# Optimization experiments

Measured on AMD Instinct MI355X. Metric: run time of the kernel, lower is better.

The kernel has to match this reference:

```python
import jax, jax.numpy as jnp
import numpy as np

N_VERTS = 500000
M_MASK = 250000
C_FEAT = 128
K_ORDER = 20000


def setup_inputs() -> dict:
    key = jax.random.key(0)
    k1, k2 = jax.random.split(key)
    img = jax.random.normal(k1, (M_MASK, C_FEAT), dtype=jnp.float32)
    # boolean mask in the original selects M_MASK rows; expressed as unique int indices
    mask_idx = jnp.arange(M_MASK, dtype=jnp.int64)
    order = jax.random.randint(k2, (2, K_ORDER), 0, N_VERTS, dtype=jnp.int64)
    return {"img": img, "mask_idx": mask_idx, "order": order, "num_vertices": N_VERTS}


def reference(img, mask_idx, order, num_vertices):
    # v_f = zeros(N, C); v_f[mask] = img
    v_f = jnp.zeros((num_vertices, img.shape[1]), dtype=img.dtype).at[mask_idx].set(img)
    # sequential copy chain, replayed in reverse column order:
    #   for idx in range(K): t = order[1, K-1-idx]; f = order[0, K-1-idx]; v_f[t] = v_f[f]
    cols = order[:, ::-1].T  # [K, 2] rows of (f, t), last column first
    def step(v, col):
        f, t = col[0], col[1]
        return v.at[t].set(v[f]), None
    v_f, _ = jax.lax.scan(step, v_f, cols)
    return v_f
```

## Files before the change

### kernel.cpp

```cpp
#include <hip/hip_runtime.h>


__global__ void init_kernel(int* __restrict__ LW, int* __restrict__ inv,
                            int* __restrict__ head, int N) {
    int r = blockIdx.x * blockDim.x + threadIdx.x;
    if (r < N) { LW[r] = -1; inv[r] = -1; head[r] = -1; }
}

__global__ void scatter_inv(const int* __restrict__ mask_idx, int* __restrict__ inv, int M) {
    int i = blockIdx.x * blockDim.x + threadIdx.x;
    if (i < M) inv[mask_idx[i]] = i;
}

__global__ void lw_chain_kernel(const int* __restrict__ order, int K,
                                int* __restrict__ LW, int* __restrict__ head,
                                int* __restrict__ next) {
    int s = blockIdx.x * blockDim.x + threadIdx.x;
    if (s < K) {
        int t = order[2 * K - 1 - s];
        atomicMax(&LW[t], s);
        next[s] = atomicExch(&head[t], s);
    }
}

__global__ void parent_kernel(const int* __restrict__ order, int K,
                              const int* __restrict__ head, const int* __restrict__ next,
                              int* __restrict__ parent) {
    int s = blockIdx.x * blockDim.x + threadIdx.x;
    if (s >= K) return;
    int f = order[K - 1 - s];
    int best = -1;
    for (int cur = head[f]; cur >= 0; cur = next[cur])
        if (cur < s && cur > best) best = cur;
    parent[s] = (best >= 0) ? best : s;
}

__global__ void res_kernel(const int* __restrict__ order, int K,
                           const int* __restrict__ parent, int* __restrict__ RES) {
    int s = blockIdx.x * blockDim.x + threadIdx.x;
    if (s >= K) return;
    int cur = s;
    int p = parent[cur];
    while (p != cur) { cur = p; p = parent[cur]; }
    RES[s] = order[K - 1 - cur];
}

__global__ void out_kernel(const float4* __restrict__ img4, const int* __restrict__ LW,
                           const int* __restrict__ inv, const int* __restrict__ RES,
                           float4* __restrict__ out4, int N, int c4shift) {
    int C4 = 1 << c4shift;
    int rowsPerBlock = blockDim.x >> c4shift;
    int row = blockIdx.x * rowsPerBlock + (threadIdx.x >> c4shift);
    int c4 = threadIdx.x & (C4 - 1);
    if (row >= N) return;
    int lw = LW[row];
    int src = (lw < 0) ? row : RES[lw];
    int j = inv[src];
    float4 val = make_float4(0.f, 0.f, 0.f, 0.f);
    if (j >= 0) val = img4[(long)j * C4 + c4];
    out4[(long)row * C4 + c4] = val;
}

extern "C" void kernel_launch(void* const* d_in, const int* in_sizes, int n_in,
                              void* d_out, int out_size, void* d_ws, size_t ws_size,
                              hipStream_t stream) {
    const float* img      = (const float*)d_in[0];
    const int*   mask_idx = (const int*)d_in[1];
    const int*   order    = (const int*)d_in[2];
    float*       out      = (float*)d_out;

    const int M  = in_sizes[1];
    const int C  = in_sizes[0] / M;
    const int K  = in_sizes[2] / 2;
    const int N  = out_size / C;
    const int C4 = C / 4;
    int c4shift = 0;
    while ((1 << c4shift) < C4) ++c4shift;

    int* LW     = (int*)d_ws;
    int* inv    = LW + N;
    int* head   = inv + N;
    int* next   = head + N;
    int* parent = next + K;
    int* RES    = parent + K;

    const int B = 256;

    init_kernel<<<(N + B - 1) / B, B, 0, stream>>>(LW, inv, head, N);
    scatter_inv<<<(M + B - 1) / B, B, 0, stream>>>(mask_idx, inv, M);
    lw_chain_kernel<<<(K + B - 1) / B, B, 0, stream>>>(order, K, LW, head, next);
    parent_kernel<<<(K + B - 1) / B, B, 0, stream>>>(order, K, head, next, parent);
    res_kernel<<<(K + B - 1) / B, B, 0, stream>>>(order, K, parent, RES);

    int rowsPerBlock = B >> c4shift;
    out_kernel<<<(N + rowsPerBlock - 1) / rowsPerBlock, B, 0, stream>>>(
        (const float4*)img, LW, inv, RES, (float4*)out, N, c4shift);
}
```

Before: 368.6 us.

## Split output into bulk stream plus sparse fix-up of copied rows

Reworks the pipeline from six kernels to four. Only the vertices touched by `order` are initialised, scatter and chain-building are fused into one kernel, and the output is first written as a plain masked copy. A sparse fix-up kernel then overwrites only the last-written target rows, walking each copy chain inline instead of building parent/RES arrays. This removes full-N passes over LW/head and the per-row LW/RES indirection in the big output kernel. In exchange, the chain resolution is redone per target in the fix-up kernel, and correctness depends on that kernel being ordered after the bulk stream.

```diff
diff --git a/kernel.cpp b/kernel.cpp
--- a/kernel.cpp
+++ b/kernel.cpp
@@ -1,64 +1,75 @@
 #include <hip/hip_runtime.h>
 
 
-__global__ void init_kernel(int* __restrict__ LW, int* __restrict__ inv,
-                            int* __restrict__ head, int N) {
-    int r = blockIdx.x * blockDim.x + threadIdx.x;
-    if (r < N) { LW[r] = -1; inv[r] = -1; head[r] = -1; }
-}
-
-__global__ void scatter_inv(const int* __restrict__ mask_idx, int* __restrict__ inv, int M) {
+__global__ __launch_bounds__(256) void k1_init(const int* __restrict__ order, int K,
+                                               int* __restrict__ inv, int* __restrict__ LW,
+                                               int* __restrict__ head, int N) {
     int i = blockIdx.x * blockDim.x + threadIdx.x;
-    if (i < M) inv[mask_idx[i]] = i;
-}
-
-__global__ void lw_chain_kernel(const int* __restrict__ order, int K,
-                                int* __restrict__ LW, int* __restrict__ head,
-                                int* __restrict__ next) {
-    int s = blockIdx.x * blockDim.x + threadIdx.x;
-    if (s < K) {
-        int t = order[2 * K - 1 - s];
-        atomicMax(&LW[t], s);
-        next[s] = atomicExch(&head[t], s);
+    if (i < N) inv[i] = -1;
+    if (i < K) {
+        int f = order[K - 1 - i];
+        int t = order[2 * K - 1 - i];
+        LW[t] = -1;
+        head[t] = -1;
+        head[f] = -1;
     }
 }
 
-__global__ void parent_kernel(const int* __restrict__ order, int K,
-                              const int* __restrict__ head, const int* __restrict__ next,
-                              int* __restrict__ parent) {
-    int s = blockIdx.x * blockDim.x + threadIdx.x;
-    if (s >= K) return;
-    int f = order[K - 1 - s];
-    int best = -1;
-    for (int cur = head[f]; cur >= 0; cur = next[cur])
-        if (cur < s && cur > best) best = cur;
-    parent[s] = (best >= 0) ? best : s;
+__global__ __launch_bounds__(256) void k2_build(const int* __restrict__ mask_idx, int M,
+                                                const int* __restrict__ order, int K,
+                                                int* __restrict__ inv, int* __restrict__ LW,
+                                                int* __restrict__ head, int* __restrict__ next) {
+    int i = blockIdx.x * blockDim.x + threadIdx.x;
+    if (i < M) inv[mask_idx[i]] = i;
+    if (i < K) {
+        int t = order[2 * K - 1 - i];
+        atomicMax(&LW[t], i);
+        next[i] = atomicExch(&head[t], i);
+    }
 }
 
-__global__ void res_kernel(const int* __restrict__ order, int K,
-                           const int* __restrict__ parent, int* __restrict__ RES) {
-    int s = blockIdx.x * blockDim.x + threadIdx.x;
-    if (s >= K) return;
-    int cur = s;
-    int p = parent[cur];
-    while (p != cur) { cur = p; p = parent[cur]; }
-    RES[s] = order[K - 1 - cur];
+__global__ __launch_bounds__(256) void k3_stream(const float4* __restrict__ img4,
+                                                 const int* __restrict__ inv,
+                                                 float4* __restrict__ out4,
+                                                 int N, int c4shift) {
+    int C4 = 1 << c4shift;
+    long idx = (long)blockIdx.x * blockDim.x + threadIdx.x;
+    long row = idx >> c4shift;
+    if (row >= N) return;
+    int c4 = (int)(idx & (C4 - 1));
+    int j = inv[(int)row];
+    float4 v = make_float4(0.f, 0.f, 0.f, 0.f);
+    if (j >= 0) v = img4[(long)j * C4 + c4];
+    out4[idx] = v;
 }
 
-__global__ void out_kernel(const float4* __restrict__ img4, const int* __restrict__ LW,
-                           const int* __restrict__ inv, const int* __restrict__ RES,
-                           float4* __restrict__ out4, int N, int c4shift) {
+__global__ __launch_bounds__(256) void k4_fix(const int* __restrict__ order, int K,
+                                              const int* __restrict__ head,
+                                              const int* __restrict__ next,
+                                              const int* __restrict__ LW,
+                                              const int* __restrict__ inv,
+                                              const float4* __restrict__ img4,
+                                              float4* __restrict__ out4, int c4shift) {
     int C4 = 1 << c4shift;
-    int rowsPerBlock = blockDim.x >> c4shift;
-    int row = blockIdx.x * rowsPerBlock + (threadIdx.x >> c4shift);
+    int perBlock = blockDim.x >> c4shift;
+    int s = blockIdx.x * perBlock + (threadIdx.x >> c4shift);
+    if (s >= K) return;
     int c4 = threadIdx.x & (C4 - 1);
-    if (row >= N) return;
-    int lw = LW[row];
-    int src = (lw < 0) ? row : RES[lw];
+    int t = order[2 * K - 1 - s];
+    if (LW[t] != s) return;
+    int cur = s, src;
+    for (;;) {
+        int f = order[K - 1 - cur];
+        int best = -1;
+        for (int nd = head[f]; nd >= 0; nd = next[nd])
+            if (nd < cur && nd > best) best = nd;
+        if (best < 0) { src = f; break; }
+        cur = best;
+    }
     int j = inv[src];
-    float4 val = make_float4(0.f, 0.f, 0.f, 0.f);
-    if (j >= 0) val = img4[(long)j * C4 + c4];
-    out4[(long)row * C4 + c4] = val;
+    float4 v = make_float4(0.f, 0.f, 0.f, 0.f);
+    if (j >= 0) v = img4[(long)j * C4 + c4];
+    out4[(long)t * C4 + c4] = v;
 }
 
 extern "C" void kernel_launch(void* const* d_in, const int* in_sizes, int n_in,
@@ -77,22 +88,23 @@
     int c4shift = 0;
     while ((1 << c4shift) < C4) ++c4shift;
 
-    int* LW     = (int*)d_ws;
-    int* inv    = LW + N;
-    int* head   = inv + N;
-    int* next   = head + N;
-    int* parent = next + K;
-    int* RES    = parent + K;
+    int* inv  = (int*)d_ws;
+    int* LW   = inv + N;
+    int* head = LW + N;
+    int* next = head + N;
 
     const int B = 256;
 
-    init_kernel<<<(N + B - 1) / B, B, 0, stream>>>(LW, inv, head, N);
-    scatter_inv<<<(M + B - 1) / B, B, 0, stream>>>(mask_idx, inv, M);
-    lw_chain_kernel<<<(K + B - 1) / B, B, 0, stream>>>(order, K, LW, head, next);
-    parent_kernel<<<(K + B - 1) / B, B, 0, stream>>>(order, K, head, next, parent);
-    res_kernel<<<(K + B - 1) / B, B, 0, stream>>>(order, K, parent, RES);
+    k1_init<<<(N + B - 1) / B, B, 0, stream>>>(order, K, inv, LW, head, N);
 
-    int rowsPerBlock = B >> c4shift;
-    out_kernel<<<(N + rowsPerBlock - 1) / rowsPerBlock, B, 0, stream>>>(
-        (const float4*)img, LW, inv, RES, (float4*)out, N, c4shift);
+    int MX = (M > K) ? M : K;
+    k2_build<<<(MX + B - 1) / B, B, 0, stream>>>(mask_idx, M, order, K, inv, LW, head, next);
+
+    long total = (long)N << c4shift;
+    k3_stream<<<(int)((total + B - 1) / B), B, 0, stream>>>(
+        (const float4*)img, inv, (float4*)out, N, c4shift);
+
+    int perBlock = B >> c4shift;
+    k4_fix<<<(K + perBlock - 1) / perBlock, B, 0, stream>>>(
+        order, K, head, next, LW, inv, (const float4*)img, (float4*)out, c4shift);
 }
```

Result: no change. 367.6 us (-0.3%).
